# Kernel tuning notes

Measured on AMD Instinct MI355X. Metric: run time of the kernel, lower is better.

## Reference

```python
import jax, jax.numpy as jnp
import numpy as np

B, T, D, H = 256, 1024, 6, 256  # batch, timesteps, per-step feature dim, hidden


def setup_inputs() -> dict:
    key = jax.random.key(0)
    ks = jax.random.split(key, 11)
    s = 1.0 / np.sqrt(H)  # torch LSTMCell/Linear default uniform init bound

    def u(k, shape):
        return jax.random.uniform(k, shape, jnp.float32, -s, s)

    return {
        "x": jax.random.normal(ks[0], (B, T * D), dtype=jnp.float32),
        "W_ih1": u(ks[1], (4 * H, D)),
        "W_hh1": u(ks[2], (4 * H, H)),
        "b_ih1": u(ks[3], (4 * H,)),
        "b_hh1": u(ks[4], (4 * H,)),
        "W_ih2": u(ks[5], (4 * H, H)),
        "W_hh2": u(ks[6], (4 * H, H)),
        "b_ih2": u(ks[7], (4 * H,)),
        "b_hh2": u(ks[8], (4 * H,)),
        "W_out": u(ks[9], (D, H)),
        "b_out": u(ks[10], (D,)),
        "future": 0,
    }


def _lstm_cell(xt, h, c, W_ih, W_hh, b_ih, b_hh):
    # gates in torch LSTMCell order: input, forget, cell(g), output
    g = xt @ W_ih.T + b_ih + h @ W_hh.T + b_hh  # [B, 4H]
    i, f, gg, o = jnp.split(g, 4, axis=-1)
    c_new = jax.nn.sigmoid(f) * c + jax.nn.sigmoid(i) * jnp.tanh(gg)
    h_new = jax.nn.sigmoid(o) * jnp.tanh(c_new)
    return h_new, c_new


def reference(x, W_ih1, W_hh1, b_ih1, b_hh1, W_ih2, W_hh2, b_ih2, b_hh2, W_out, b_out, future):
    # future must be 0 (the future>0 branch in the original module is unrunnable).
    b = x.shape[0]
    h = W_hh1.shape[1]
    t = x.shape[1] // D
    xs = x.reshape(b, t, D).transpose(1, 0, 2)  # [T, B, D]

    def step(carry, xt):
        h1, c1, h2, c2 = carry
        h1, c1 = _lstm_cell(xt, h1, c1, W_ih1, W_hh1, b_ih1, b_hh1)
        h2, c2 = _lstm_cell(h1, h2, c2, W_ih2, W_hh2, b_ih2, b_hh2)
        out = h2 @ W_out.T + b_out  # [B, D]
        return (h1, c1, h2, c2), out

    z = jnp.zeros((b, h), dtype=jnp.float32)
    _, outs = jax.lax.scan(step, (z, z, z, z), xs)  # outs: [T, B, D]
    # torch.cat(outputs, dim=1) -> [B, T*D]
    return outs.transpose(1, 0, 2).reshape(b, t * D)
```

## Files before the change

### kernel.cpp

```cpp
#include <hip/hip_runtime.h>

#define BB 256
#define TT 1024
#define DDIM 6
#define HH 256
#define AGSCOPE __HIP_MEMORY_SCOPE_AGENT

typedef float  f4v __attribute__((ext_vector_type(4)));
typedef float  f2v __attribute__((ext_vector_type(2)));
typedef short  s8v __attribute__((ext_vector_type(8)));
typedef unsigned int u32;


__device__ __forceinline__ float sigf(float x) {
    return __builtin_amdgcn_rcpf(1.0f + __expf(-x));
}
__device__ __forceinline__ float tanhf_fast(float x) {
    return fmaf(2.0f, __builtin_amdgcn_rcpf(1.0f + __expf(-2.0f * x)), -1.0f);
}
__device__ __forceinline__ void st_agent_u16(unsigned short* p, unsigned short v) {
    __hip_atomic_store(p, v, __ATOMIC_RELAXED, AGSCOPE);
}

#define MFMA(a, b, c) __builtin_amdgcn_mfma_f32_16x16x32_bf16(a, b, c, 0, 0, 0)

__device__ __forceinline__ void cvt_hl(float v, unsigned short& hi, unsigned short& lo) {
    u32 u = __float_as_uint(v);
    u32 r = (u + 0x7fffu + ((u >> 16) & 1u)) & 0xffff0000u;
    hi = (unsigned short)(r >> 16);
    float lof = v - __uint_as_float(r);
    u32 u2 = __float_as_uint(lof);
    lo = (unsigned short)((u2 + 0x7fffu + ((u2 >> 16) & 1u)) >> 16);
}

__device__ __forceinline__ void pack8_hl(const float* __restrict__ p, s8v& hi, s8v& lo) {
    #pragma unroll
    for (int j = 0; j < 8; ++j) {
        unsigned short h, l;
        cvt_hl(p[j], h, l);
        hi[j] = (short)h;
        lo[j] = (short)l;
    }
}

__device__ __forceinline__ void stage16(const unsigned short* g, unsigned short* lds) {
    __builtin_amdgcn_global_load_lds(
        (const __attribute__((address_space(1))) u32*)g,
        (__attribute__((address_space(3))) u32*)lds, 16, 0, 17);
}

__device__ __forceinline__ void group_barrier(int* flags, int bg, int token) {
    __syncthreads();
    asm volatile("" ::: "memory");
    if (threadIdx.x == 0) {
        __hip_atomic_store(&flags[blockIdx.x], token, __ATOMIC_RELAXED, AGSCOPE);
    }
    if (threadIdx.x < 32) {
        while (__hip_atomic_load(&flags[bg + 8 * (int)threadIdx.x], __ATOMIC_RELAXED,
                                 AGSCOPE) < token) {
            __builtin_amdgcn_s_sleep(1);
        }
    }
    __syncthreads();
    asm volatile("" ::: "memory");
}

__device__ __forceinline__ void emit_out(float hval,
                                         const float (*Wo)[256],
                                         float (*redsc)[8],
                                         float boV,
                                         float* __restrict__ op, int tid) {
    float p0 = Wo[0][tid] * hval;
    float p1 = Wo[1][tid] * hval;
    float p2 = Wo[2][tid] * hval;
    float p3 = Wo[3][tid] * hval;
    float p4 = Wo[4][tid] * hval;
    float p5 = Wo[5][tid] * hval;
    #pragma unroll
    for (int off = 1; off < 64; off <<= 1) {
        p0 += __shfl_xor(p0, off);
        p1 += __shfl_xor(p1, off);
        p2 += __shfl_xor(p2, off);
        p3 += __shfl_xor(p3, off);
        p4 += __shfl_xor(p4, off);
        p5 += __shfl_xor(p5, off);
    }
    const int wid = tid >> 6;
    if ((tid & 63) == 0) {
        redsc[wid][0] = p0; redsc[wid][1] = p1; redsc[wid][2] = p2;
        redsc[wid][3] = p3; redsc[wid][4] = p4; redsc[wid][5] = p5;
    }
    __syncthreads();
    if (tid < 6) {
        op[tid] = redsc[0][tid] + redsc[1][tid] + redsc[2][tid] + redsc[3][tid] + boV;
    }
}

__global__ __launch_bounds__(256, 1) void lstm_persist(
    const float* __restrict__ x,
    const float* __restrict__ W_ih1, const float* __restrict__ W_hh1,
    const float* __restrict__ b_ih1, const float* __restrict__ b_hh1,
    const float* __restrict__ W_ih2, const float* __restrict__ W_hh2,
    const float* __restrict__ b_ih2, const float* __restrict__ b_hh2,
    const float* __restrict__ W_out, const float* __restrict__ b_out,
    float* __restrict__ out,
    int* __restrict__ flags,
    unsigned short* __restrict__ B1h, unsigned short* __restrict__ B1l,
    unsigned short* __restrict__ B2h, unsigned short* __restrict__ B2l)
{
    __shared__ unsigned short sB1h[2][8][64][8];
    __shared__ unsigned short sB1l[2][8][64][8];
    __shared__ unsigned short sB2h[2][8][64][8];
    __shared__ unsigned short sB2l[2][8][64][8];
    __shared__ float Wo[6][256];
    __shared__ float redsc[4][8];

    const int tid = threadIdx.x;
    const int bg  = blockIdx.x & 7;
    const int gg  = blockIdx.x >> 3;
    const int wid = tid >> 6;
    const int l   = tid & 63;
    const int gh  = wid >> 1;
    const int bh  = wid & 1;
    const int kl  = (l >> 4) << 3;
    const int r32  = (gh << 4) + (l & 15);
    const int gr_a = (r32 & 3) * HH + (gg << 3) + (r32 >> 2);
    const int du       = (gh << 2) + (l >> 4);
    const int db       = (bh << 4) + (l & 15);
    const int unit_abs = (gg << 3) + du;
    const int db_abs   = (bg << 5) + db;
    const int ro       = (bg << 5) + gg;

    const int so_base = bh * 4096 + (gg >> 2) * 512 + (gg & 3) * 128 + (l & 15) * 8 + du;
    const int eo = ((gg >> 4) * 4096) + ((tid >> 5) * 512) + (((tid >> 3) & 3) * 128)
                 + ((gg & 15) * 8) + (tid & 7);

    for (int i = tid; i < 4096; i += 256) {
        ((u32*)sB1h)[i] = 0u; ((u32*)sB1l)[i] = 0u;
        ((u32*)sB2h)[i] = 0u; ((u32*)sB2l)[i] = 0u;
    }
    for (int i = tid; i < 6 * 256; i += 256) Wo[i >> 8][i & 255] = W_out[i];

    s8v A1h[8], A1l[8], A2h[16], A2l[16];
    {
        const float* w1 = W_hh1 + gr_a * HH;
        #pragma unroll
        for (int c = 0; c < 8; ++c) pack8_hl(w1 + c * 32 + kl, A1h[c], A1l[c]);
        const float* w2i = W_ih2 + gr_a * HH;
        #pragma unroll
        for (int c = 0; c < 8; ++c) pack8_hl(w2i + c * 32 + kl, A2h[c], A2l[c]);
        const float* w2h = W_hh2 + gr_a * HH;
        #pragma unroll
        for (int c = 0; c < 8; ++c) pack8_hl(w2h + c * 32 + kl, A2h[8 + c], A2l[8 + c]);
    }

    float b1a[4], b2a[4], Wxr[4][6];
    #pragma unroll
    for (int g = 0; g < 4; ++g) {
        const int gr = g * HH + unit_abs;
        b1a[g] = b_ih1[gr] + b_hh1[gr];
        b2a[g] = b_ih2[gr] + b_hh2[gr];
        #pragma unroll
        for (int d = 0; d < 6; ++d) Wxr[g][d] = W_ih1[gr * DDIM + d];
    }
    const float boV = (tid < 6) ? b_out[tid] : 0.0f;
    float c1 = 0.0f, c2 = 0.0f;

    const float* xbase = x + (size_t)db_abs * (TT * DDIM);
    f2v xA = *(const f2v*)(xbase);
    f2v xB = *(const f2v*)(xbase + 2);
    f2v xC = *(const f2v*)(xbase + 4);
    __syncthreads();

    #pragma unroll 1
    for (int t = 0; t < TT; ++t) {
        const int cur = t & 1, prv = cur ^ 1;

        f4v aA = {0.f,0.f,0.f,0.f}, aB = {0.f,0.f,0.f,0.f}, aC = {0.f,0.f,0.f,0.f};
        #pragma unroll
        for (int c = 0; c < 8; ++c) {
            const s8v vhi = *(const s8v*)&sB1h[bh][c][l][0];
            const s8v vlo = *(const s8v*)&sB1l[bh][c][l][0];
            aA = MFMA(A1h[c], vhi, aA);
            aB = MFMA(A1h[c], vlo, aB);
            aC = MFMA(A1l[c], vhi, aC);
        }
        {
            const f4v acc = (aA + aB) + aC;
            float ga[4];
            #pragma unroll
            for (int g = 0; g < 4; ++g) {
                float a = acc[g] + b1a[g];
                a = fmaf(Wxr[g][0], xA.x, a); a = fmaf(Wxr[g][1], xA.y, a);
                a = fmaf(Wxr[g][2], xB.x, a); a = fmaf(Wxr[g][3], xB.y, a);
                a = fmaf(Wxr[g][4], xC.x, a); a = fmaf(Wxr[g][5], xC.y, a);
                ga[g] = a;
            }
            const float i1 = sigf(ga[0]), f1 = sigf(ga[1]);
            const float g1 = tanhf_fast(ga[2]), o1 = sigf(ga[3]);
            c1 = fmaf(f1, c1, i1 * g1);
            const float h1v = o1 * tanhf_fast(c1);
            unsigned short hh, hl;
            cvt_hl(h1v, hh, hl);
            const int i1x = (cur * 8 + bg) * 8192 + so_base;
            st_agent_u16(&B1h[i1x], hh);
            st_agent_u16(&B1l[i1x], hl);
        }

        group_barrier(flags, bg, t + 1);

        if (wid == 0) {
            const unsigned short* g = B1h + (cur * 8 + bg) * 8192;
            #pragma unroll
            for (int i = 0; i < 16; ++i) stage16(g + i * 512 + l * 8, &sB1h[0][0][0][0] + i * 512);
        } else if (wid == 1) {
            const unsigned short* g = B1l + (cur * 8 + bg) * 8192;
            #pragma unroll
            for (int i = 0; i < 16; ++i) stage16(g + i * 512 + l * 8, &sB1l[0][0][0][0] + i * 512);
        } else if (wid == 2) {
            if (t > 0) {
                const unsigned short* g = B2h + (prv * 8 + bg) * 8192;
                #pragma unroll
                for (int i = 0; i < 16; ++i) stage16(g + i * 512 + l * 8, &sB2h[0][0][0][0] + i * 512);
            }
        } else {
            if (t > 0) {
                const unsigned short* g = B2l + (prv * 8 + bg) * 8192;
                #pragma unroll
                for (int i = 0; i < 16; ++i) stage16(g + i * 512 + l * 8, &sB2l[0][0][0][0] + i * 512);
            }
        }

        const float* xnp = xbase + ((t + 1 < TT) ? (t + 1) : t) * DDIM;
        const f2v xAn = *(const f2v*)(xnp);
        const f2v xBn = *(const f2v*)(xnp + 2);
        const f2v xCn = *(const f2v*)(xnp + 4);

        __syncthreads();

        if (t > 0) {
            const float hval =
                __uint_as_float((u32)(((const unsigned short*)sB2h)[eo]) << 16)
              + __uint_as_float((u32)(((const unsigned short*)sB2l)[eo]) << 16);
            emit_out(hval, Wo, redsc, boV, out + ro * (TT * DDIM) + (t - 1) * DDIM, tid);
        }

        f4v eA = {0.f,0.f,0.f,0.f}, eB = {0.f,0.f,0.f,0.f}, eC = {0.f,0.f,0.f,0.f};
        #pragma unroll
        for (int c = 0; c < 8; ++c) {
            const s8v vhi = *(const s8v*)&sB1h[bh][c][l][0];
            const s8v vlo = *(const s8v*)&sB1l[bh][c][l][0];
            eA = MFMA(A2h[c], vhi, eA);
            eB = MFMA(A2h[c], vlo, eB);
            eC = MFMA(A2l[c], vhi, eC);
        }
        #pragma unroll
        for (int c = 0; c < 8; ++c) {
            const s8v vhi = *(const s8v*)&sB2h[bh][c][l][0];
            const s8v vlo = *(const s8v*)&sB2l[bh][c][l][0];
            eA = MFMA(A2h[8 + c], vhi, eA);
            eB = MFMA(A2h[8 + c], vlo, eB);
            eC = MFMA(A2l[8 + c], vhi, eC);
        }
        {
            const f4v acc2 = (eA + eB) + eC;
            const float i2  = sigf(acc2[0] + b2a[0]);
            const float f2g = sigf(acc2[1] + b2a[1]);
            const float g2  = tanhf_fast(acc2[2] + b2a[2]);
            const float o2  = sigf(acc2[3] + b2a[3]);
            c2 = fmaf(f2g, c2, i2 * g2);
            const float h2v = o2 * tanhf_fast(c2);
            unsigned short hh, hl;
            cvt_hl(h2v, hh, hl);
            const int i2x = (cur * 8 + bg) * 8192 + so_base;
            st_agent_u16(&B2h[i2x], hh);
            st_agent_u16(&B2l[i2x], hl);
        }

        xA = xAn; xB = xBn; xC = xCn;
    }

    group_barrier(flags, bg, TT + 1);
    {
        const int curF = (TT - 1) & 1;
        if (wid == 2) {
            const unsigned short* g = B2h + (curF * 8 + bg) * 8192;
            #pragma unroll
            for (int i = 0; i < 16; ++i) stage16(g + i * 512 + l * 8, &sB2h[0][0][0][0] + i * 512);
        } else if (wid == 3) {
            const unsigned short* g = B2l + (curF * 8 + bg) * 8192;
            #pragma unroll
            for (int i = 0; i < 16; ++i) stage16(g + i * 512 + l * 8, &sB2l[0][0][0][0] + i * 512);
        }
        __syncthreads();
        const float hval =
            __uint_as_float((u32)(((const unsigned short*)sB2h)[eo]) << 16)
          + __uint_as_float((u32)(((const unsigned short*)sB2l)[eo]) << 16);
        emit_out(hval, Wo, redsc, boV, out + ro * (TT * DDIM) + (TT - 1) * DDIM, tid);
    }
}

extern "C" void kernel_launch(void* const* d_in, const int* in_sizes, int n_in,
                              void* d_out, int out_size, void* d_ws, size_t ws_size,
                              hipStream_t stream) {
    (void)in_sizes; (void)n_in; (void)out_size; (void)ws_size;
    const float* x     = (const float*)d_in[0];
    const float* W_ih1 = (const float*)d_in[1];
    const float* W_hh1 = (const float*)d_in[2];
    const float* b_ih1 = (const float*)d_in[3];
    const float* b_hh1 = (const float*)d_in[4];
    const float* W_ih2 = (const float*)d_in[5];
    const float* W_hh2 = (const float*)d_in[6];
    const float* b_ih2 = (const float*)d_in[7];
    const float* b_hh2 = (const float*)d_in[8];
    const float* W_out = (const float*)d_in[9];
    const float* b_out = (const float*)d_in[10];
    float* out = (float*)d_out;

    char* ws = (char*)d_ws;
    int* flags = (int*)ws;
    unsigned short* B1h = (unsigned short*)(ws + 1024);
    unsigned short* B1l = (unsigned short*)(ws + 1024 + 262144);
    unsigned short* B2h = (unsigned short*)(ws + 1024 + 524288);
    unsigned short* B2l = (unsigned short*)(ws + 1024 + 786432);

    hipMemsetAsync(d_ws, 0, 1024, stream);

    hipLaunchKernelGGL(lstm_persist, dim3(256), dim3(256), 0, stream,
                       x, W_ih1, W_hh1, b_ih1, b_hh1,
                       W_ih2, W_hh2, b_ih2, b_hh2,
                       W_out, b_out, out, flags, B1h, B1l, B2h, B2l);
}
```

Measured before the change: 6.287 ms.

## Split batch into 16 groups, split K across waves, switch to fp16 hi/lo MFMA

Raises the grid from 256 to 512 blocks by splitting the batch into 16 groups of 16 rows. Inside a block, the two wave halves now divide the reduction (K) dimension and combine partial sums through shared memory with extra __syncthreads. The bf16 hi/lo split becomes an fp16 hi/lo split with a scaled low part, and the layer-2 low-part weights move to LDS to cut register pressure so two blocks can fit per CU. The goal is shorter per-block MFMA chains per timestep. In exchange it adds intra-block syncs, wider group barriers, and a change in numerical precision.

```diff
diff --git a/kernel.cpp b/kernel.cpp
--- a/kernel.cpp
+++ b/kernel.cpp
@@ -1,14 +1,15 @@
 #include <hip/hip_runtime.h>
 
-#define BB 256
 #define TT 1024
 #define DDIM 6
 #define HH 256
 #define AGSCOPE __HIP_MEMORY_SCOPE_AGENT
-
-typedef float  f4v __attribute__((ext_vector_type(4)));
-typedef float  f2v __attribute__((ext_vector_type(2)));
-typedef short  s8v __attribute__((ext_vector_type(8)));
+#define LOSC 4.8828125e-4f
+
+typedef float    f4v __attribute__((ext_vector_type(4)));
+typedef float    f2v __attribute__((ext_vector_type(2)));
+typedef _Float16 hf;
+typedef hf       h8v __attribute__((ext_vector_type(8)));
 typedef unsigned int u32;
 
 
@@ -22,24 +23,19 @@
     __hip_atomic_store(p, v, __ATOMIC_RELAXED, AGSCOPE);
 }
 
-#define MFMA(a, b, c) __builtin_amdgcn_mfma_f32_16x16x32_bf16(a, b, c, 0, 0, 0)
-
-__device__ __forceinline__ void cvt_hl(float v, unsigned short& hi, unsigned short& lo) {
-    u32 u = __float_as_uint(v);
-    u32 r = (u + 0x7fffu + ((u >> 16) & 1u)) & 0xffff0000u;
-    hi = (unsigned short)(r >> 16);
-    float lof = v - __uint_as_float(r);
-    u32 u2 = __float_as_uint(lof);
-    lo = (unsigned short)((u2 + 0x7fffu + ((u2 >> 16) & 1u)) >> 16);
-}
-
-__device__ __forceinline__ void pack8_hl(const float* __restrict__ p, s8v& hi, s8v& lo) {
+#define MFMA(a, b, c) __builtin_amdgcn_mfma_f32_16x16x32_f16(a, b, c, 0, 0, 0)
+
+__device__ __forceinline__ void cvt_hl(float v, hf& hi, hf& lo) {
+    hi = (hf)v;
+    lo = (hf)((v - (float)hi) * 2048.0f);
+}
+__device__ __forceinline__ void pack8_hl(const float* __restrict__ p, h8v& hi, h8v& lo) {
     #pragma unroll
     for (int j = 0; j < 8; ++j) {
-        unsigned short h, l;
+        hf h, l;
         cvt_hl(p[j], h, l);
-        hi[j] = (short)h;
-        lo[j] = (short)l;
+        hi[j] = h;
+        lo[j] = l;
     }
 }
 
@@ -56,7 +52,7 @@
         __hip_atomic_store(&flags[blockIdx.x], token, __ATOMIC_RELAXED, AGSCOPE);
     }
     if (threadIdx.x < 32) {
-        while (__hip_atomic_load(&flags[bg + 8 * (int)threadIdx.x], __ATOMIC_RELAXED,
+        while (__hip_atomic_load(&flags[(bg << 5) + (int)threadIdx.x], __ATOMIC_RELAXED,
                                  AGSCOPE) < token) {
             __builtin_amdgcn_s_sleep(1);
         }
@@ -96,7 +92,7 @@
     }
 }
 
-__global__ __launch_bounds__(256, 1) void lstm_persist(
+__global__ __launch_bounds__(256, 2) void lstm_persist(
     const float* __restrict__ x,
     const float* __restrict__ W_ih1, const float* __restrict__ W_hh1,
     const float* __restrict__ b_ih1, const float* __restrict__ b_hh1,
@@ -108,68 +104,79 @@
     unsigned short* __restrict__ B1h, unsigned short* __restrict__ B1l,
     unsigned short* __restrict__ B2h, unsigned short* __restrict__ B2l)
 {
-    __shared__ unsigned short sB1h[2][8][64][8];
-    __shared__ unsigned short sB1l[2][8][64][8];
-    __shared__ unsigned short sB2h[2][8][64][8];
-    __shared__ unsigned short sB2l[2][8][64][8];
+    __shared__ unsigned short sB1h[8][64][8], sB1l[8][64][8];
+    __shared__ unsigned short sB2h[8][64][8], sB2l[8][64][8];
+    __shared__ hf    sA2l[4][8][64][8];
+    __shared__ float sWx[4][8][8];
     __shared__ float Wo[6][256];
     __shared__ float redsc[4][8];
+    __shared__ f4v pscrA[2][64], pscrB[2][64];
 
     const int tid = threadIdx.x;
-    const int bg  = blockIdx.x & 7;
-    const int gg  = blockIdx.x >> 3;
+    const int blk = blockIdx.x;
+    const int gg  = blk & 31;
+    const int bg  = blk >> 5;
     const int wid = tid >> 6;
     const int l   = tid & 63;
     const int gh  = wid >> 1;
-    const int bh  = wid & 1;
+    const int kh  = wid & 1;
     const int kl  = (l >> 4) << 3;
     const int r32  = (gh << 4) + (l & 15);
     const int gr_a = (r32 & 3) * HH + (gg << 3) + (r32 >> 2);
     const int du       = (gh << 2) + (l >> 4);
-    const int db       = (bh << 4) + (l & 15);
+    const int db       = l & 15;
     const int unit_abs = (gg << 3) + du;
-    const int db_abs   = (bg << 5) + db;
-    const int ro       = (bg << 5) + gg;
-
-    const int so_base = bh * 4096 + (gg >> 2) * 512 + (gg & 3) * 128 + (l & 15) * 8 + du;
-    const int eo = ((gg >> 4) * 4096) + ((tid >> 5) * 512) + (((tid >> 3) & 3) * 128)
-                 + ((gg & 15) * 8) + (tid & 7);
-
-    for (int i = tid; i < 4096; i += 256) {
+    const int db_abs   = (bg << 4) + db;
+    const int ro       = (bg << 4) + (gg & 15);
+
+    const int so_base = (unit_abs >> 5) * 512 + ((unit_abs >> 3) & 3) * 128
+                      + db * 8 + (unit_abs & 7);
+    const int eo = (tid >> 5) * 512 + (((tid >> 3) & 3) * 128) + (gg & 15) * 8 + (tid & 7);
+
+    for (int i = tid; i < 2048; i += 256) {
         ((u32*)sB1h)[i] = 0u; ((u32*)sB1l)[i] = 0u;
         ((u32*)sB2h)[i] = 0u; ((u32*)sB2l)[i] = 0u;
     }
     for (int i = tid; i < 6 * 256; i += 256) Wo[i >> 8][i & 255] = W_out[i];
-
-    s8v A1h[8], A1l[8], A2h[16], A2l[16];
+    for (int i = tid; i < 192; i += 256) {
+        const int r = i / 6, d = i - r * 6;
+        sWx[r >> 3][r & 7][d] = W_ih1[((r >> 3) * HH + (gg << 3) + (r & 7)) * DDIM + d];
+    }
+
+    h8v A1h[4], A1l[4], A2h[8];
+    #pragma unroll
+    for (int c = 0; c < 4; ++c) {
+        const int cc = (kh << 2) + c;
+        pack8_hl(W_hh1 + gr_a * HH + cc * 32 + kl, A1h[c], A1l[c]);
+    }
     {
-        const float* w1 = W_hh1 + gr_a * HH;
+        const float* W2 = kh ? W_hh2 : W_ih2;
         #pragma unroll
-        for (int c = 0; c < 8; ++c) pack8_hl(w1 + c * 32 + kl, A1h[c], A1l[c]);
-        const float* w2i = W_ih2 + gr_a * HH;
-        #pragma unroll
-        for (int c = 0; c < 8; ++c) pack8_hl(w2i + c * 32 + kl, A2h[c], A2l[c]);
-        const float* w2h = W_hh2 + gr_a * HH;
-        #pragma unroll
-        for (int c = 0; c < 8; ++c) pack8_hl(w2h + c * 32 + kl, A2h[8 + c], A2l[8 + c]);
-    }
-
-    float b1a[4], b2a[4], Wxr[4][6];
+        for (int c = 0; c < 8; ++c) {
+            h8v hi, lo;
+            pack8_hl(W2 + gr_a * HH + c * 32 + kl, hi, lo);
+            A2h[c] = hi;
+            *(h8v*)&sA2l[wid][c][l][0] = lo;
+        }
+    }
+
+    float b1a[4], b2a[4];
     #pragma unroll
     for (int g = 0; g < 4; ++g) {
         const int gr = g * HH + unit_abs;
         b1a[g] = b_ih1[gr] + b_hh1[gr];
         b2a[g] = b_ih2[gr] + b_hh2[gr];
-        #pragma unroll
-        for (int d = 0; d < 6; ++d) Wxr[g][d] = W_ih1[gr * DDIM + d];
     }
     const float boV = (tid < 6) ? b_out[tid] : 0.0f;
     float c1 = 0.0f, c2 = 0.0f;
 
     const float* xbase = x + (size_t)db_abs * (TT * DDIM);
-    f2v xA = *(const f2v*)(xbase);
-    f2v xB = *(const f2v*)(xbase + 2);
-    f2v xC = *(const f2v*)(xbase + 4);
+    f2v xA = {0.f,0.f}, xB = {0.f,0.f}, xC = {0.f,0.f};
+    if (kh == 0) {
+        xA = *(const f2v*)(xbase);
+        xB = *(const f2v*)(xbase + 2);
+        xC = *(const f2v*)(xbase + 4);
+    }
     __syncthreads();
 
     #pragma unroll 1
@@ -178,103 +185,112 @@
 
         f4v aA = {0.f,0.f,0.f,0.f}, aB = {0.f,0.f,0.f,0.f}, aC = {0.f,0.f,0.f,0.f};
         #pragma unroll
-        for (int c = 0; c < 8; ++c) {
-            const s8v vhi = *(const s8v*)&sB1h[bh][c][l][0];
-            const s8v vlo = *(const s8v*)&sB1l[bh][c][l][0];
+        for (int c = 0; c < 4; ++c) {
+            const int cc = (kh << 2) + c;
+            const h8v vhi = *(const h8v*)&sB1h[cc][l][0];
+            const h8v vlo = *(const h8v*)&sB1l[cc][l][0];
             aA = MFMA(A1h[c], vhi, aA);
             aB = MFMA(A1h[c], vlo, aB);
             aC = MFMA(A1l[c], vhi, aC);
         }
         {
-            const f4v acc = (aA + aB) + aC;
-            float ga[4];
-            #pragma unroll
-            for (int g = 0; g < 4; ++g) {
-                float a = acc[g] + b1a[g];
-                a = fmaf(Wxr[g][0], xA.x, a); a = fmaf(Wxr[g][1], xA.y, a);
-                a = fmaf(Wxr[g][2], xB.x, a); a = fmaf(Wxr[g][3], xB.y, a);
-                a = fmaf(Wxr[g][4], xC.x, a); a = fmaf(Wxr[g][5], xC.y, a);
-                ga[g] = a;
-            }
-            const float i1 = sigf(ga[0]), f1 = sigf(ga[1]);
-            const float g1 = tanhf_fast(ga[2]), o1 = sigf(ga[3]);
-            c1 = fmaf(f1, c1, i1 * g1);
-            const float h1v = o1 * tanhf_fast(c1);
-            unsigned short hh, hl;
-            cvt_hl(h1v, hh, hl);
-            const int i1x = (cur * 8 + bg) * 8192 + so_base;
-            st_agent_u16(&B1h[i1x], hh);
-            st_agent_u16(&B1l[i1x], hl);
+            const f4v p1 = aA + (aB + aC) * LOSC;
+            if (kh) pscrA[gh][l] = p1;
+            __syncthreads();
+            if (!kh) {
+                const f4v acc = p1 + pscrA[gh][l];
+                float ga[4];
+                #pragma unroll
+                for (int g = 0; g < 4; ++g) {
+                    float a = acc[g] + b1a[g];
+                    a = fmaf(sWx[g][du][0], xA.x, a); a = fmaf(sWx[g][du][1], xA.y, a);
+                    a = fmaf(sWx[g][du][2], xB.x, a); a = fmaf(sWx[g][du][3], xB.y, a);
+                    a = fmaf(sWx[g][du][4], xC.x, a); a = fmaf(sWx[g][du][5], xC.y, a);
+                    ga[g] = a;
+                }
+                const float i1 = sigf(ga[0]), f1 = sigf(ga[1]);
+                const float g1 = tanhf_fast(ga[2]), o1 = sigf(ga[3]);
+                c1 = fmaf(f1, c1, i1 * g1);
+                const float h1v = o1 * tanhf_fast(c1);
+                hf hh, hl;
+                cvt_hl(h1v, hh, hl);
+                const int idx = (cur * 16 + bg) * 4096 + so_base;
+                st_agent_u16(&B1h[idx], __builtin_bit_cast(unsigned short, hh));
+                st_agent_u16(&B1l[idx], __builtin_bit_cast(unsigned short, hl));
+            }
         }
 
         group_barrier(flags, bg, t + 1);
 
         if (wid == 0) {
-            const unsigned short* g = B1h + (cur * 8 + bg) * 8192;
-            #pragma unroll
-            for (int i = 0; i < 16; ++i) stage16(g + i * 512 + l * 8, &sB1h[0][0][0][0] + i * 512);
+            const unsigned short* g = B1h + (cur * 16 + bg) * 4096;
+            #pragma unroll
+            for (int i = 0; i < 8; ++i) stage16(g + i * 512 + l * 8, &sB1h[0][0][0] + i * 512);
         } else if (wid == 1) {
-            const unsigned short* g = B1l + (cur * 8 + bg) * 8192;
-            #pragma unroll
-            for (int i = 0; i < 16; ++i) stage16(g + i * 512 + l * 8, &sB1l[0][0][0][0] + i * 512);
+            const unsigned short* g = B1l + (cur * 16 + bg) * 4096;
+            #pragma unroll
+            for (int i = 0; i < 8; ++i) stage16(g + i * 512 + l * 8, &sB1l[0][0][0] + i * 512);
         } else if (wid == 2) {
             if (t > 0) {
-                const unsigned short* g = B2h + (prv * 8 + bg) * 8192;
+                const unsigned short* g = B2h + (prv * 16 + bg) * 4096;
                 #pragma unroll
-                for (int i = 0; i < 16; ++i) stage16(g + i * 512 + l * 8, &sB2h[0][0][0][0] + i * 512);
+                for (int i = 0; i < 8; ++i) stage16(g + i * 512 + l * 8, &sB2h[0][0][0] + i * 512);
             }
         } else {
             if (t > 0) {
-                const unsigned short* g = B2l + (prv * 8 + bg) * 8192;
+                const unsigned short* g = B2l + (prv * 16 + bg) * 4096;
                 #pragma unroll
-                for (int i = 0; i < 16; ++i) stage16(g + i * 512 + l * 8, &sB2l[0][0][0][0] + i * 512);
-            }
-        }
-
-        const float* xnp = xbase + ((t + 1 < TT) ? (t + 1) : t) * DDIM;
-        const f2v xAn = *(const f2v*)(xnp);
-        const f2v xBn = *(const f2v*)(xnp + 2);
-        const f2v xCn = *(const f2v*)(xnp + 4);
+                for (int i = 0; i < 8; ++i) stage16(g + i * 512 + l * 8, &sB2l[0][0][0] + i * 512);
+            }
+        }
+
+        f2v xAn = xA, xBn = xB, xCn = xC;
+        if (kh == 0 && t + 1 < TT) {
+            const float* xnp = xbase + (t + 1) * DDIM;
+            xAn = *(const f2v*)(xnp);
+            xBn = *(const f2v*)(xnp + 2);
+            xCn = *(const f2v*)(xnp + 4);
+        }
 
         __syncthreads();
 
-        if (t > 0) {
-            const float hval =
-                __uint_as_float((u32)(((const unsigned short*)sB2h)[eo]) << 16)
-              + __uint_as_float((u32)(((const unsigned short*)sB2l)[eo]) << 16);
+        if (gg < 16 && t > 0) {
+            const hf ehi = __builtin_bit_cast(hf, ((const unsigned short*)sB2h)[eo]);
+            const hf elo = __builtin_bit_cast(hf, ((const unsigned short*)sB2l)[eo]);
+            const float hval = (float)ehi + LOSC * (float)elo;
             emit_out(hval, Wo, redsc, boV, out + ro * (TT * DDIM) + (t - 1) * DDIM, tid);
         }
 
-        f4v eA = {0.f,0.f,0.f,0.f}, eB = {0.f,0.f,0.f,0.f}, eC = {0.f,0.f,0.f,0.f};
-        #pragma unroll
-        for (int c = 0; c < 8; ++c) {
-            const s8v vhi = *(const s8v*)&sB1h[bh][c][l][0];
-            const s8v vlo = *(const s8v*)&sB1l[bh][c][l][0];
-            eA = MFMA(A2h[c], vhi, eA);
-            eB = MFMA(A2h[c], vlo, eB);
-            eC = MFMA(A2l[c], vhi, eC);
-        }
-        #pragma unroll
-        for (int c = 0; c < 8; ++c) {
-            const s8v vhi = *(const s8v*)&sB2h[bh][c][l][0];
-            const s8v vlo = *(const s8v*)&sB2l[bh][c][l][0];
-            eA = MFMA(A2h[8 + c], vhi, eA);
-            eB = MFMA(A2h[8 + c], vlo, eB);
-            eC = MFMA(A2l[8 + c], vhi, eC);
-        }
         {
-            const f4v acc2 = (eA + eB) + eC;
-            const float i2  = sigf(acc2[0] + b2a[0]);
-            const float f2g = sigf(acc2[1] + b2a[1]);
-            const float g2  = tanhf_fast(acc2[2] + b2a[2]);
-            const float o2  = sigf(acc2[3] + b2a[3]);
-            c2 = fmaf(f2g, c2, i2 * g2);
-            const float h2v = o2 * tanhf_fast(c2);
-            unsigned short hh, hl;
-            cvt_hl(h2v, hh, hl);
-            const int i2x = (cur * 8 + bg) * 8192 + so_base;
-            st_agent_u16(&B2h[i2x], hh);
-            st_agent_u16(&B2l[i2x], hl);
+            const unsigned short* shp = kh ? &sB2h[0][0][0] : &sB1h[0][0][0];
+            const unsigned short* slp = kh ? &sB2l[0][0][0] : &sB1l[0][0][0];
+            f4v eA = {0.f,0.f,0.f,0.f}, eB = {0.f,0.f,0.f,0.f}, eC = {0.f,0.f,0.f,0.f};
+            #pragma unroll
+            for (int c = 0; c < 8; ++c) {
+                const h8v vhi = *(const h8v*)(shp + c * 512 + l * 8);
+                const h8v vlo = *(const h8v*)(slp + c * 512 + l * 8);
+                const h8v Al  = *(const h8v*)&sA2l[wid][c][l][0];
+                eA = MFMA(A2h[c], vhi, eA);
+                eB = MFMA(A2h[c], vlo, eB);
+                eC = MFMA(Al,     vhi, eC);
+            }
+            const f4v p5 = eA + (eB + eC) * LOSC;
+            if (kh) pscrB[gh][l] = p5;
+            __syncthreads();
+            if (!kh) {
+                const f4v acc2 = p5 + pscrB[gh][l];
+                const float i2  = sigf(acc2[0] + b2a[0]);
+                const float f2g = sigf(acc2[1] + b2a[1]);
+                const float g2  = tanhf_fast(acc2[2] + b2a[2]);
+                const float o2  = sigf(acc2[3] + b2a[3]);
+                c2 = fmaf(f2g, c2, i2 * g2);
+                const float h2v = o2 * tanhf_fast(c2);
+                hf hh, hl;
+                cvt_hl(h2v, hh, hl);
+                const int idx = (cur * 16 + bg) * 4096 + so_base;
+                st_agent_u16(&B2h[idx], __builtin_bit_cast(unsigned short, hh));
+                st_agent_u16(&B2l[idx], __builtin_bit_cast(unsigned short, hl));
+            }
         }
 
         xA = xAn; xB = xBn; xC = xCn;
@@ -284,19 +300,21 @@
     {
         const int curF = (TT - 1) & 1;
         if (wid == 2) {
-            const unsigned short* g = B2h + (curF * 8 + bg) * 8192;
-            #pragma unroll
-            for (int i = 0; i < 16; ++i) stage16(g + i * 512 + l * 8, &sB2h[0][0][0][0] + i * 512);
+            const unsigned short* g = B2h + (curF * 16 + bg) * 4096;
+            #pragma unroll
+            for (int i = 0; i < 8; ++i) stage16(g + i * 512 + l * 8, &sB2h[0][0][0] + i * 512);
         } else if (wid == 3) {
-            const unsigned short* g = B2l + (curF * 8 + bg) * 8192;
-            #pragma unroll
-            for (int i = 0; i < 16; ++i) stage16(g + i * 512 + l * 8, &sB2l[0][0][0][0] + i * 512);
+            const unsigned short* g = B2l + (curF * 16 + bg) * 4096;
+            #pragma unroll
+            for (int i = 0; i < 8; ++i) stage16(g + i * 512 + l * 8, &sB2l[0][0][0] + i * 512);
         }
         __syncthreads();
-        const float hval =
-            __uint_as_float((u32)(((const unsigned short*)sB2h)[eo]) << 16)
-          + __uint_as_float((u32)(((const unsigned short*)sB2l)[eo]) << 16);
-        emit_out(hval, Wo, redsc, boV, out + ro * (TT * DDIM) + (TT - 1) * DDIM, tid);
+        if (gg < 16) {
+            const hf ehi = __builtin_bit_cast(hf, ((const unsigned short*)sB2h)[eo]);
+            const hf elo = __builtin_bit_cast(hf, ((const unsigned short*)sB2l)[eo]);
+            const float hval = (float)ehi + LOSC * (float)elo;
+            emit_out(hval, Wo, redsc, boV, out + ro * (TT * DDIM) + (TT - 1) * DDIM, tid);
+        }
     }
 }
 
@@ -319,14 +337,14 @@
 
     char* ws = (char*)d_ws;
     int* flags = (int*)ws;
-    unsigned short* B1h = (unsigned short*)(ws + 1024);
-    unsigned short* B1l = (unsigned short*)(ws + 1024 + 262144);
-    unsigned short* B2h = (unsigned short*)(ws + 1024 + 524288);
-    unsigned short* B2l = (unsigned short*)(ws + 1024 + 786432);
-
-    hipMemsetAsync(d_ws, 0, 1024, stream);
-
-    hipLaunchKernelGGL(lstm_persist, dim3(256), dim3(256), 0, stream,
+    unsigned short* B1h = (unsigned short*)(ws + 2048);
+    unsigned short* B1l = (unsigned short*)(ws + 2048 + 262144);
+    unsigned short* B2h = (unsigned short*)(ws + 2048 + 524288);
+    unsigned short* B2l = (unsigned short*)(ws + 2048 + 786432);
+
+    hipMemsetAsync(d_ws, 0, 2048, stream);
+
+    hipLaunchKernelGGL(lstm_persist, dim3(512), dim3(256), 0, stream,
                        x, W_ih1, W_hh1, b_ih1, b_hh1,
                        W_ih2, W_hh2, b_ih2, b_hh2,
                        W_out, b_out, out, flags, B1h, B1l, B2h, B2l);
```

Measured after the change: 5.255 ms, median of 2. 1.2x faster.

## Split LSTM across 1024 workgroups with per-wave hi/lo MFMA split

Applied to the files above, without the earlier changes.

Repartitions the persistent LSTM from 256 workgroups of 256 threads to 1024 workgroups of 192 threads, with 3 resident per CU. Each workgroup now handles 16 batch rows and 4 hidden units. The three bf16 split-precision MFMA products (hi*hi, hi*lo, lo*hi) move onto three separate waves and are reduced through LDS, so each wave makes a single MFMA chain. The group barrier widens to 64 participants per batch group using u16 flags, and the output projection reads W_out from global memory on only 16 workgroups. This is meant to spread the serial per-step work across more CUs and shorten each wave's MFMA chain. In exchange it adds LDS reductions, extra __syncthreads, and a wider cross-workgroup barrier on every step.

```diff
diff --git a/kernel.cpp b/kernel.cpp
--- a/kernel.cpp
+++ b/kernel.cpp
@@ -1,15 +1,15 @@
 #include <hip/hip_runtime.h>
 
-#define BB 256
 #define TT 1024
 #define DDIM 6
 #define HH 256
 #define AGSCOPE __HIP_MEMORY_SCOPE_AGENT
 
-typedef float  f4v __attribute__((ext_vector_type(4)));
-typedef float  f2v __attribute__((ext_vector_type(2)));
-typedef short  s8v __attribute__((ext_vector_type(8)));
+typedef float f4v __attribute__((ext_vector_type(4)));
+typedef float f2v __attribute__((ext_vector_type(2)));
+typedef short s8v __attribute__((ext_vector_type(8)));
 typedef unsigned int u32;
+typedef unsigned short u16;
 
 
 __device__ __forceinline__ float sigf(float x) {
@@ -18,46 +18,45 @@
 __device__ __forceinline__ float tanhf_fast(float x) {
     return fmaf(2.0f, __builtin_amdgcn_rcpf(1.0f + __expf(-2.0f * x)), -1.0f);
 }
-__device__ __forceinline__ void st_agent_u16(unsigned short* p, unsigned short v) {
+__device__ __forceinline__ void st_agent_u16(u16* p, u16 v) {
     __hip_atomic_store(p, v, __ATOMIC_RELAXED, AGSCOPE);
 }
 
 #define MFMA(a, b, c) __builtin_amdgcn_mfma_f32_16x16x32_bf16(a, b, c, 0, 0, 0)
 
-__device__ __forceinline__ void cvt_hl(float v, unsigned short& hi, unsigned short& lo) {
+__device__ __forceinline__ void cvt_hl(float v, u16& hi, u16& lo) {
     u32 u = __float_as_uint(v);
     u32 r = (u + 0x7fffu + ((u >> 16) & 1u)) & 0xffff0000u;
-    hi = (unsigned short)(r >> 16);
+    hi = (u16)(r >> 16);
     float lof = v - __uint_as_float(r);
     u32 u2 = __float_as_uint(lof);
-    lo = (unsigned short)((u2 + 0x7fffu + ((u2 >> 16) & 1u)) >> 16);
-}
-
+    lo = (u16)((u2 + 0x7fffu + ((u2 >> 16) & 1u)) >> 16);
+}
 __device__ __forceinline__ void pack8_hl(const float* __restrict__ p, s8v& hi, s8v& lo) {
     #pragma unroll
     for (int j = 0; j < 8; ++j) {
-        unsigned short h, l;
+        u16 h, l;
         cvt_hl(p[j], h, l);
         hi[j] = (short)h;
         lo[j] = (short)l;
     }
 }
 
-__device__ __forceinline__ void stage16(const unsigned short* g, unsigned short* lds) {
+__device__ __forceinline__ void stage16(const u16* g, u16* lds) {
     __builtin_amdgcn_global_load_lds(
         (const __attribute__((address_space(1))) u32*)g,
         (__attribute__((address_space(3))) u32*)lds, 16, 0, 17);
 }
 
-__device__ __forceinline__ void group_barrier(int* flags, int bg, int token) {
+__device__ __forceinline__ void group_barrier(u16* flags, int bg, int token) {
     __syncthreads();
     asm volatile("" ::: "memory");
     if (threadIdx.x == 0) {
-        __hip_atomic_store(&flags[blockIdx.x], token, __ATOMIC_RELAXED, AGSCOPE);
-    }
-    if (threadIdx.x < 32) {
-        while (__hip_atomic_load(&flags[bg + 8 * (int)threadIdx.x], __ATOMIC_RELAXED,
-                                 AGSCOPE) < token) {
+        __hip_atomic_store(&flags[blockIdx.x], (u16)token, __ATOMIC_RELAXED, AGSCOPE);
+    }
+    if (threadIdx.x < 64) {
+        while ((int)__hip_atomic_load(&flags[(bg << 6) + (int)threadIdx.x], __ATOMIC_RELAXED,
+                                      AGSCOPE) < token) {
             __builtin_amdgcn_s_sleep(1);
         }
     }
@@ -65,38 +64,34 @@
     asm volatile("" ::: "memory");
 }
 
-__device__ __forceinline__ void emit_out(float hval,
-                                         const float (*Wo)[256],
-                                         float (*redsc)[8],
-                                         float boV,
-                                         float* __restrict__ op, int tid) {
-    float p0 = Wo[0][tid] * hval;
-    float p1 = Wo[1][tid] * hval;
-    float p2 = Wo[2][tid] * hval;
-    float p3 = Wo[3][tid] * hval;
-    float p4 = Wo[4][tid] * hval;
-    float p5 = Wo[5][tid] * hval;
-    #pragma unroll
-    for (int off = 1; off < 64; off <<= 1) {
-        p0 += __shfl_xor(p0, off);
-        p1 += __shfl_xor(p1, off);
-        p2 += __shfl_xor(p2, off);
-        p3 += __shfl_xor(p3, off);
-        p4 += __shfl_xor(p4, off);
-        p5 += __shfl_xor(p5, off);
-    }
-    const int wid = tid >> 6;
-    if ((tid & 63) == 0) {
-        redsc[wid][0] = p0; redsc[wid][1] = p1; redsc[wid][2] = p2;
-        redsc[wid][3] = p3; redsc[wid][4] = p4; redsc[wid][5] = p5;
+__device__ __forceinline__ void emit_outg(float h0, float h1v,
+                                          const float* __restrict__ W_out,
+                                          float (*redsc)[8],
+                                          float boV,
+                                          float* __restrict__ op, int tid) {
+    float p[6];
+    if (tid < 128) {
+        #pragma unroll
+        for (int d = 0; d < 6; ++d) {
+            p[d] = W_out[d * HH + tid] * h0 + W_out[d * HH + tid + 128] * h1v;
+        }
+        #pragma unroll
+        for (int off = 1; off < 64; off <<= 1) {
+            #pragma unroll
+            for (int d = 0; d < 6; ++d) p[d] += __shfl_xor(p[d], off);
+        }
+        if ((tid & 63) == 0) {
+            #pragma unroll
+            for (int d = 0; d < 6; ++d) redsc[tid >> 6][d] = p[d];
+        }
     }
     __syncthreads();
     if (tid < 6) {
-        op[tid] = redsc[0][tid] + redsc[1][tid] + redsc[2][tid] + redsc[3][tid] + boV;
-    }
-}
-
-__global__ __launch_bounds__(256, 1) void lstm_persist(
+        op[tid] = redsc[0][tid] + redsc[1][tid] + boV;
+    }
+}
+
+__global__ __launch_bounds__(192, 3) void lstm_persist(
     const float* __restrict__ x,
     const float* __restrict__ W_ih1, const float* __restrict__ W_hh1,
     const float* __restrict__ b_ih1, const float* __restrict__ b_hh1,
@@ -104,199 +99,203 @@
     const float* __restrict__ b_ih2, const float* __restrict__ b_hh2,
     const float* __restrict__ W_out, const float* __restrict__ b_out,
     float* __restrict__ out,
-    int* __restrict__ flags,
-    unsigned short* __restrict__ B1h, unsigned short* __restrict__ B1l,
-    unsigned short* __restrict__ B2h, unsigned short* __restrict__ B2l)
+    u16* __restrict__ flags,
+    u16* __restrict__ B1h, u16* __restrict__ B1l,
+    u16* __restrict__ B2h, u16* __restrict__ B2l)
 {
-    __shared__ unsigned short sB1h[2][8][64][8];
-    __shared__ unsigned short sB1l[2][8][64][8];
-    __shared__ unsigned short sB2h[2][8][64][8];
-    __shared__ unsigned short sB2l[2][8][64][8];
-    __shared__ float Wo[6][256];
-    __shared__ float redsc[4][8];
+    __shared__ u16 sB1h[8][64][8], sB1l[8][64][8];
+    __shared__ u16 sB2h[8][64][8], sB2l[8][64][8];
+    __shared__ f4v pscr1[2][64], pscr5[2][64];
+    __shared__ float redsc[2][8];
 
     const int tid = threadIdx.x;
-    const int bg  = blockIdx.x & 7;
-    const int gg  = blockIdx.x >> 3;
+    const int blk = blockIdx.x;
+    const int bg  = blk >> 6;
+    const int gy  = blk & 63;
     const int wid = tid >> 6;
     const int l   = tid & 63;
-    const int gh  = wid >> 1;
-    const int bh  = wid & 1;
     const int kl  = (l >> 4) << 3;
-    const int r32  = (gh << 4) + (l & 15);
-    const int gr_a = (r32 & 3) * HH + (gg << 3) + (r32 >> 2);
-    const int du       = (gh << 2) + (l >> 4);
-    const int db       = (bh << 4) + (l & 15);
-    const int unit_abs = (gg << 3) + du;
-    const int db_abs   = (bg << 5) + db;
-    const int ro       = (bg << 5) + gg;
-
-    const int so_base = bh * 4096 + (gg >> 2) * 512 + (gg & 3) * 128 + (l & 15) * 8 + du;
-    const int eo = ((gg >> 4) * 4096) + ((tid >> 5) * 512) + (((tid >> 3) & 3) * 128)
-                 + ((gg & 15) * 8) + (tid & 7);
-
-    for (int i = tid; i < 4096; i += 256) {
+    const int r16  = l & 15;
+    const int gr_a = (r16 & 3) * HH + (gy << 2) + (r16 >> 2);
+    const int du       = l >> 4;
+    const int db       = l & 15;
+    const int unit_abs = (gy << 2) + du;
+    const int db_abs   = (bg << 4) + db;
+    const bool emitWG  = (gy < 16);
+    const int ro       = (bg << 4) + gy;
+
+    const int so_base = (unit_abs >> 5) * 512 + ((unit_abs >> 3) & 3) * 128
+                      + db * 8 + (unit_abs & 7);
+    const int eo0 = (tid >> 5) * 512 + (((tid >> 3) & 3) * 128) + gy * 8 + (tid & 7);
+    const int u1  = tid + 128;
+    const int eo1 = (u1 >> 5) * 512 + (((u1 >> 3) & 3) * 128) + gy * 8 + (u1 & 7);
+
+    for (int i = tid; i < 2048; i += 192) {
         ((u32*)sB1h)[i] = 0u; ((u32*)sB1l)[i] = 0u;
         ((u32*)sB2h)[i] = 0u; ((u32*)sB2l)[i] = 0u;
     }
-    for (int i = tid; i < 6 * 256; i += 256) Wo[i >> 8][i & 255] = W_out[i];
-
-    s8v A1h[8], A1l[8], A2h[16], A2l[16];
-    {
-        const float* w1 = W_hh1 + gr_a * HH;
-        #pragma unroll
-        for (int c = 0; c < 8; ++c) pack8_hl(w1 + c * 32 + kl, A1h[c], A1l[c]);
-        const float* w2i = W_ih2 + gr_a * HH;
-        #pragma unroll
-        for (int c = 0; c < 8; ++c) pack8_hl(w2i + c * 32 + kl, A2h[c], A2l[c]);
-        const float* w2h = W_hh2 + gr_a * HH;
-        #pragma unroll
-        for (int c = 0; c < 8; ++c) pack8_hl(w2h + c * 32 + kl, A2h[8 + c], A2l[8 + c]);
-    }
+
+    s8v P1f[8], P5f[16];
+    #pragma unroll
+    for (int c = 0; c < 8; ++c) {
+        s8v hi, lo;
+        pack8_hl(W_hh1 + gr_a * HH + c * 32 + kl, hi, lo);
+        P1f[c] = (wid == 2) ? lo : hi;
+    }
+    #pragma unroll
+    for (int c = 0; c < 8; ++c) {
+        s8v hi, lo;
+        pack8_hl(W_ih2 + gr_a * HH + c * 32 + kl, hi, lo);
+        P5f[c] = (wid == 2) ? lo : hi;
+    }
+    #pragma unroll
+    for (int c = 0; c < 8; ++c) {
+        s8v hi, lo;
+        pack8_hl(W_hh2 + gr_a * HH + c * 32 + kl, hi, lo);
+        P5f[8 + c] = (wid == 2) ? lo : hi;
+    }
+    const u16* sb1B = (wid == 1) ? &sB1l[0][0][0] : &sB1h[0][0][0];
+    const u16* sb2B = (wid == 1) ? &sB2l[0][0][0] : &sB2h[0][0][0];
 
     float b1a[4], b2a[4], Wxr[4][6];
-    #pragma unroll
-    for (int g = 0; g < 4; ++g) {
-        const int gr = g * HH + unit_abs;
-        b1a[g] = b_ih1[gr] + b_hh1[gr];
-        b2a[g] = b_ih2[gr] + b_hh2[gr];
-        #pragma unroll
-        for (int d = 0; d < 6; ++d) Wxr[g][d] = W_ih1[gr * DDIM + d];
+    float c1 = 0.0f, c2 = 0.0f;
+    f2v xA = {0.f, 0.f}, xB = {0.f, 0.f}, xC = {0.f, 0.f};
+    const float* xbase = x + (size_t)db_abs * (TT * DDIM);
+    if (wid == 0) {
+        #pragma unroll
+        for (int g = 0; g < 4; ++g) {
+            const int gr = g * HH + unit_abs;
+            b1a[g] = b_ih1[gr] + b_hh1[gr];
+            b2a[g] = b_ih2[gr] + b_hh2[gr];
+            #pragma unroll
+            for (int d = 0; d < 6; ++d) Wxr[g][d] = W_ih1[gr * DDIM + d];
+        }
+        xA = *(const f2v*)(xbase);
+        xB = *(const f2v*)(xbase + 2);
+        xC = *(const f2v*)(xbase + 4);
     }
     const float boV = (tid < 6) ? b_out[tid] : 0.0f;
-    float c1 = 0.0f, c2 = 0.0f;
-
-    const float* xbase = x + (size_t)db_abs * (TT * DDIM);
-    f2v xA = *(const f2v*)(xbase);
-    f2v xB = *(const f2v*)(xbase + 2);
-    f2v xC = *(const f2v*)(xbase + 4);
     __syncthreads();
 
     #pragma unroll 1
     for (int t = 0; t < TT; ++t) {
         const int cur = t & 1, prv = cur ^ 1;
 
-        f4v aA = {0.f,0.f,0.f,0.f}, aB = {0.f,0.f,0.f,0.f}, aC = {0.f,0.f,0.f,0.f};
+        f4v a = {0.f, 0.f, 0.f, 0.f};
         #pragma unroll
         for (int c = 0; c < 8; ++c) {
-            const s8v vhi = *(const s8v*)&sB1h[bh][c][l][0];
-            const s8v vlo = *(const s8v*)&sB1l[bh][c][l][0];
-            aA = MFMA(A1h[c], vhi, aA);
-            aB = MFMA(A1h[c], vlo, aB);
-            aC = MFMA(A1l[c], vhi, aC);
-        }
-        {
-            const f4v acc = (aA + aB) + aC;
+            const s8v v = *(const s8v*)(sb1B + c * 512 + l * 8);
+            a = MFMA(P1f[c], v, a);
+        }
+        if (wid) pscr1[wid - 1][l] = a;
+        __syncthreads();
+        if (wid == 0) {
+            const f4v acc = (a + pscr1[0][l]) + pscr1[1][l];
             float ga[4];
             #pragma unroll
             for (int g = 0; g < 4; ++g) {
-                float a = acc[g] + b1a[g];
-                a = fmaf(Wxr[g][0], xA.x, a); a = fmaf(Wxr[g][1], xA.y, a);
-                a = fmaf(Wxr[g][2], xB.x, a); a = fmaf(Wxr[g][3], xB.y, a);
-                a = fmaf(Wxr[g][4], xC.x, a); a = fmaf(Wxr[g][5], xC.y, a);
-                ga[g] = a;
+                float v = acc[g] + b1a[g];
+                v = fmaf(Wxr[g][0], xA.x, v); v = fmaf(Wxr[g][1], xA.y, v);
+                v = fmaf(Wxr[g][2], xB.x, v); v = fmaf(Wxr[g][3], xB.y, v);
+                v = fmaf(Wxr[g][4], xC.x, v); v = fmaf(Wxr[g][5], xC.y, v);
+                ga[g] = v;
             }
             const float i1 = sigf(ga[0]), f1 = sigf(ga[1]);
             const float g1 = tanhf_fast(ga[2]), o1 = sigf(ga[3]);
             c1 = fmaf(f1, c1, i1 * g1);
             const float h1v = o1 * tanhf_fast(c1);
-            unsigned short hh, hl;
+            u16 hh, hl;
             cvt_hl(h1v, hh, hl);
-            const int i1x = (cur * 8 + bg) * 8192 + so_base;
-            st_agent_u16(&B1h[i1x], hh);
-            st_agent_u16(&B1l[i1x], hl);
+            const int idx = (cur * 16 + bg) * 4096 + so_base;
+            st_agent_u16(&B1h[idx], hh);
+            st_agent_u16(&B1l[idx], hl);
         }
 
         group_barrier(flags, bg, t + 1);
 
         if (wid == 0) {
-            const unsigned short* g = B1h + (cur * 8 + bg) * 8192;
-            #pragma unroll
-            for (int i = 0; i < 16; ++i) stage16(g + i * 512 + l * 8, &sB1h[0][0][0][0] + i * 512);
+            const u16* g = B1h + (cur * 16 + bg) * 4096;
+            #pragma unroll
+            for (int i = 0; i < 8; ++i) stage16(g + i * 512 + l * 8, &sB1h[0][0][0] + i * 512);
         } else if (wid == 1) {
-            const unsigned short* g = B1l + (cur * 8 + bg) * 8192;
-            #pragma unroll
-            for (int i = 0; i < 16; ++i) stage16(g + i * 512 + l * 8, &sB1l[0][0][0][0] + i * 512);
-        } else if (wid == 2) {
-            if (t > 0) {
-                const unsigned short* g = B2h + (prv * 8 + bg) * 8192;
-                #pragma unroll
-                for (int i = 0; i < 16; ++i) stage16(g + i * 512 + l * 8, &sB2h[0][0][0][0] + i * 512);
-            }
-        } else {
-            if (t > 0) {
-                const unsigned short* g = B2l + (prv * 8 + bg) * 8192;
-                #pragma unroll
-                for (int i = 0; i < 16; ++i) stage16(g + i * 512 + l * 8, &sB2l[0][0][0][0] + i * 512);
-            }
-        }
-
-        const float* xnp = xbase + ((t + 1 < TT) ? (t + 1) : t) * DDIM;
-        const f2v xAn = *(const f2v*)(xnp);
-        const f2v xBn = *(const f2v*)(xnp + 2);
-        const f2v xCn = *(const f2v*)(xnp + 4);
+            const u16* g = B1l + (cur * 16 + bg) * 4096;
+            #pragma unroll
+            for (int i = 0; i < 8; ++i) stage16(g + i * 512 + l * 8, &sB1l[0][0][0] + i * 512);
+        } else if (t > 0) {
+            const u16* gh2 = B2h + (prv * 16 + bg) * 4096;
+            const u16* gl2 = B2l + (prv * 16 + bg) * 4096;
+            #pragma unroll
+            for (int i = 0; i < 8; ++i) stage16(gh2 + i * 512 + l * 8, &sB2h[0][0][0] + i * 512);
+            #pragma unroll
+            for (int i = 0; i < 8; ++i) stage16(gl2 + i * 512 + l * 8, &sB2l[0][0][0] + i * 512);
+        }
+
+        if (wid == 0 && t + 1 < TT) {
+            const float* xnp = xbase + (t + 1) * DDIM;
+            xA = *(const f2v*)(xnp);
+            xB = *(const f2v*)(xnp + 2);
+            xC = *(const f2v*)(xnp + 4);
+        }
 
         __syncthreads();
 
-        if (t > 0) {
-            const float hval =
-                __uint_as_float((u32)(((const unsigned short*)sB2h)[eo]) << 16)
-              + __uint_as_float((u32)(((const unsigned short*)sB2l)[eo]) << 16);
-            emit_out(hval, Wo, redsc, boV, out + ro * (TT * DDIM) + (t - 1) * DDIM, tid);
-        }
-
-        f4v eA = {0.f,0.f,0.f,0.f}, eB = {0.f,0.f,0.f,0.f}, eC = {0.f,0.f,0.f,0.f};
+        if (emitWG && t > 0) {
+            const float h0 = __uint_as_float((u32)(((const u16*)sB2h)[eo0]) << 16)
+                           + __uint_as_float((u32)(((const u16*)sB2l)[eo0]) << 16);
+            const float h1v = __uint_as_float((u32)(((const u16*)sB2h)[eo1]) << 16)
+                            + __uint_as_float((u32)(((const u16*)sB2l)[eo1]) << 16);
+            emit_outg(h0, h1v, W_out, redsc, boV, out + ro * (TT * DDIM) + (t - 1) * DDIM, tid);
+        }
+
+        f4v e = {0.f, 0.f, 0.f, 0.f};
         #pragma unroll
         for (int c = 0; c < 8; ++c) {
-            const s8v vhi = *(const s8v*)&sB1h[bh][c][l][0];
-            const s8v vlo = *(const s8v*)&sB1l[bh][c][l][0];
-            eA = MFMA(A2h[c], vhi, eA);
-            eB = MFMA(A2h[c], vlo, eB);
-            eC = MFMA(A2l[c], vhi, eC);
+            const s8v v = *(const s8v*)(sb1B + c * 512 + l * 8);
+            e = MFMA(P5f[c], v, e);
         }
         #pragma unroll
         for (int c = 0; c < 8; ++c) {
-            const s8v vhi = *(const s8v*)&sB2h[bh][c][l][0];
-            const s8v vlo = *(const s8v*)&sB2l[bh][c][l][0];
-            eA = MFMA(A2h[8 + c], vhi, eA);
-            eB = MFMA(A2h[8 + c], vlo, eB);
-            eC = MFMA(A2l[8 + c], vhi, eC);
-        }
-        {
-            const f4v acc2 = (eA + eB) + eC;
+            const s8v v = *(const s8v*)(sb2B + c * 512 + l * 8);
+            e = MFMA(P5f[8 + c], v, e);
+        }
+        if (wid) pscr5[wid - 1][l] = e;
+        __syncthreads();
+        if (wid == 0) {
+            const f4v acc2 = (e + pscr5[0][l]) + pscr5[1][l];
             const float i2  = sigf(acc2[0] + b2a[0]);
             const float f2g = sigf(acc2[1] + b2a[1]);
             const float g2  = tanhf_fast(acc2[2] + b2a[2]);
             const float o2  = sigf(acc2[3] + b2a[3]);
             c2 = fmaf(f2g, c2, i2 * g2);
             const float h2v = o2 * tanhf_fast(c2);
-            unsigned short hh, hl;
+            u16 hh, hl;
             cvt_hl(h2v, hh, hl);
-            const int i2x = (cur * 8 + bg) * 8192 + so_base;
-            st_agent_u16(&B2h[i2x], hh);
-            st_agent_u16(&B2l[i2x], hl);
-        }
-
-        xA = xAn; xB = xBn; xC = xCn;
+            const int idx = (cur * 16 + bg) * 4096 + so_base;
+            st_agent_u16(&B2h[idx], hh);
+            st_agent_u16(&B2l[idx], hl);
+        }
     }
 
     group_barrier(flags, bg, TT + 1);
     {
         const int curF = (TT - 1) & 1;
-        if (wid == 2) {
-            const unsigned short* g = B2h + (curF * 8 + bg) * 8192;
-            #pragma unroll
-            for (int i = 0; i < 16; ++i) stage16(g + i * 512 + l * 8, &sB2h[0][0][0][0] + i * 512);
-        } else if (wid == 3) {
-            const unsigned short* g = B2l + (curF * 8 + bg) * 8192;
-            #pragma unroll
-            for (int i = 0; i < 16; ++i) stage16(g + i * 512 + l * 8, &sB2l[0][0][0][0] + i * 512);
+        if (wid == 0) {
+            const u16* g = B2h + (curF * 16 + bg) * 4096;
+            #pragma unroll
+            for (int i = 0; i < 8; ++i) stage16(g + i * 512 + l * 8, &sB2h[0][0][0] + i * 512);
+        } else if (wid == 1) {
+            const u16* g = B2l + (curF * 16 + bg) * 4096;
+            #pragma unroll
+            for (int i = 0; i < 8; ++i) stage16(g + i * 512 + l * 8, &sB2l[0][0][0] + i * 512);
         }
         __syncthreads();
-        const float hval =
-            __uint_as_float((u32)(((const unsigned short*)sB2h)[eo]) << 16)
-          + __uint_as_float((u32)(((const unsigned short*)sB2l)[eo]) << 16);
-        emit_out(hval, Wo, redsc, boV, out + ro * (TT * DDIM) + (TT - 1) * DDIM, tid);
+        if (emitWG) {
+            const float h0 = __uint_as_float((u32)(((const u16*)sB2h)[eo0]) << 16)
+                           + __uint_as_float((u32)(((const u16*)sB2l)[eo0]) << 16);
+            const float h1v = __uint_as_float((u32)(((const u16*)sB2h)[eo1]) << 16)
+                            + __uint_as_float((u32)(((const u16*)sB2l)[eo1]) << 16);
+            emit_outg(h0, h1v, W_out, redsc, boV, out + ro * (TT * DDIM) + (TT - 1) * DDIM, tid);
+        }
     }
 }
 
@@ -318,15 +317,15 @@
     float* out = (float*)d_out;
 
     char* ws = (char*)d_ws;
-    int* flags = (int*)ws;
-    unsigned short* B1h = (unsigned short*)(ws + 1024);
-    unsigned short* B1l = (unsigned short*)(ws + 1024 + 262144);
-    unsigned short* B2h = (unsigned short*)(ws + 1024 + 524288);
-    unsigned short* B2l = (unsigned short*)(ws + 1024 + 786432);
-
-    hipMemsetAsync(d_ws, 0, 1024, stream);
-
-    hipLaunchKernelGGL(lstm_persist, dim3(256), dim3(256), 0, stream,
+    u16* flags = (u16*)ws;
+    u16* B1h = (u16*)(ws + 2048);
+    u16* B1l = (u16*)(ws + 2048 + 262144);
+    u16* B2h = (u16*)(ws + 2048 + 524288);
+    u16* B2l = (u16*)(ws + 2048 + 786432);
+
+    hipMemsetAsync(d_ws, 0, 2048, stream);
+
+    hipLaunchKernelGGL(lstm_persist, dim3(1024), dim3(192), 0, stream,
                        x, W_ih1, W_hh1, b_ih1, b_hh1,
                        W_ih2, W_hh2, b_ih2, b_hh2,
                        W_out, b_out, out, flags, B1h, B1l, B2h, B2l);
```

New measurement: 14.66 ms. 2.33x slower.
